# Kernel tuning notes

Measured on AMD Instinct MI355X. Metric: run time of the kernel, lower is better.

## Reference

```python
import jax, jax.numpy as jnp
import numpy as np

E, H, I = 5, 768, 1024  # num_experts, hidden_dim, intermediate_dim
TOP_K = 2


def setup_inputs() -> dict:
    key = jax.random.key(0)
    ks = jax.random.split(key, 6)
    s = 0.02
    return {
        "x": jax.random.normal(ks[0], (4, 2048, H), dtype=jnp.float32),
        "router_w": jax.random.normal(ks[1], (E, H), dtype=jnp.float32) * s,  # torch Linear (out,in)
        "router_b": jnp.zeros((E,), dtype=jnp.float32),
        "gate_w": jax.random.normal(ks[2], (E, H, I), dtype=jnp.float32) * s,
        "up_w": jax.random.normal(ks[3], (E, H, I), dtype=jnp.float32) * s,
        "down_w": jax.random.normal(ks[4], (E, I, H), dtype=jnp.float32) * s,
    }


def reference(x, router_w, router_b, gate_w, up_w, down_w):
    B, S, Hd = x.shape
    xf = x.reshape(-1, Hd)                       # [T, H]
    T = xf.shape[0]
    # Router: linear (with bias) -> softmax -> top-2 -> renormalize
    logits = xf @ router_w.T + router_b          # [T, E]
    scores = jax.nn.softmax(logits, axis=-1)
    vals, idx = jax.lax.top_k(scores, TOP_K)     # [T, 2]
    vals = vals / jnp.sum(vals, axis=-1, keepdims=True)
    # Dense combine weights: zero for unselected experts (same math as the
    # per-expert gather/scatter loop in the original module).
    comb = jnp.zeros((T, gate_w.shape[0]), dtype=x.dtype)
    comb = comb.at[jnp.arange(T)[:, None], idx].add(vals)  # [T, E]
    # SwiGLU per expert, vectorized over experts
    g = jnp.einsum('th,ehi->tei', xf, gate_w)    # [T, E, I]
    u = jnp.einsum('th,ehi->tei', xf, up_w)
    y = jnp.einsum('tei,eih->teh', jax.nn.silu(g) * u, down_w)  # [T, E, H]
    out = jnp.einsum('teh,te->th', y, comb)
    return out.reshape(B, S, Hd)
```

## Files before the change

### kernel.cpp

```cpp
#include <hip/hip_runtime.h>
#include <hip/hip_bf16.h>
#include <cstdint>
#include <cstddef>

#define T_TOK 8192
#define H_DIM 768
#define I_DIM 1024
#define N_EXP 5
#define MAXTILE 136

typedef short v8s __attribute__((ext_vector_type(8)));
typedef float v4f __attribute__((ext_vector_type(4)));

static __device__ __forceinline__ unsigned short f2bf(float f) {
    union { float f; unsigned int u; } v; v.f = f;
    unsigned int u = v.u;
    unsigned int r = (u + 0x7fffu + ((u >> 16) & 1u)) >> 16;
    return (unsigned short)r;
}
static __device__ __forceinline__ float bf2f(unsigned short s) {
    union { unsigned int u; float f; } v; v.u = ((unsigned int)s) << 16; return v.f;
}

static __device__ __forceinline__ void async16(const unsigned short* g, unsigned short* l) {
    __builtin_amdgcn_global_load_lds(
        (const __attribute__((address_space(1))) unsigned int*)g,
        (__attribute__((address_space(3))) unsigned int*)l, 16, 0, 0);
}

__global__ void k_prep(const float* __restrict__ gw, const float* __restrict__ uw,
                       const float* __restrict__ dw,
                       unsigned short* __restrict__ wbt, unsigned short* __restrict__ dbt,
                       const float* __restrict__ x, const float* __restrict__ rw,
                       const float* __restrict__ rb, unsigned short* __restrict__ xb,
                       int* __restrict__ top2e, float2* __restrict__ top2w) {
    const int z = blockIdx.z;
    const int tid = threadIdx.x;
    if (z < 3 * N_EXP) {
        __shared__ float tile[64][65];
        const int lrow = tid >> 4;
        const int lcol = (tid & 15) * 4;
        const int ocol = tid >> 2;
        const int seg = tid & 3;
        if (z < 2 * N_EXP) {
            if (blockIdx.y >= H_DIM / 64) return;
            const int e = z % N_EXP;
            const int isUp = z >= N_EXP;
            const float* src = (isUp ? uw : gw) + (size_t)e * H_DIM * I_DIM;
            const int c0 = blockIdx.x * 64, r0 = blockIdx.y * 64;
#pragma unroll
            for (int i = 0; i < 4; i++) {
                float4 v = *(const float4*)(src + (size_t)(r0 + i * 16 + lrow) * I_DIM + c0 + lcol);
                tile[i * 16 + lrow][lcol + 0] = v.x; tile[i * 16 + lrow][lcol + 1] = v.y;
                tile[i * 16 + lrow][lcol + 2] = v.z; tile[i * 16 + lrow][lcol + 3] = v.w;
            }
            __syncthreads();
            const int c = c0 + ocol;
            const int orow = (c >> 4) * 32 + (c & 15) + (isUp ? 16 : 0);
            unsigned short* dst = wbt + ((size_t)e * 2 * I_DIM + orow) * H_DIM + r0 + seg * 16;
#pragma unroll
            for (int q = 0; q < 4; q++) {
                ushort4 o;
                o.x = f2bf(tile[seg * 16 + q * 4 + 0][ocol]);
                o.y = f2bf(tile[seg * 16 + q * 4 + 1][ocol]);
                o.z = f2bf(tile[seg * 16 + q * 4 + 2][ocol]);
                o.w = f2bf(tile[seg * 16 + q * 4 + 3][ocol]);
                *(ushort4*)(dst + q * 4) = o;
            }
        } else {
            if (blockIdx.x >= H_DIM / 64) return;
            const int e = z - 2 * N_EXP;
            const float* src = dw + (size_t)e * I_DIM * H_DIM;
            unsigned short* dstb = dbt + (size_t)e * I_DIM * H_DIM;
            const int c0 = blockIdx.x * 64, r0 = blockIdx.y * 64;
#pragma unroll
            for (int i = 0; i < 4; i++) {
                float4 v = *(const float4*)(src + (size_t)(r0 + i * 16 + lrow) * H_DIM + c0 + lcol);
                tile[i * 16 + lrow][lcol + 0] = v.x; tile[i * 16 + lrow][lcol + 1] = v.y;
                tile[i * 16 + lrow][lcol + 2] = v.z; tile[i * 16 + lrow][lcol + 3] = v.w;
            }
            __syncthreads();
            const int c = c0 + ocol;
            unsigned short* dst = dstb + (size_t)c * I_DIM + r0 + seg * 16;
#pragma unroll
            for (int q = 0; q < 4; q++) {
                ushort4 o;
                o.x = f2bf(tile[seg * 16 + q * 4 + 0][ocol]);
                o.y = f2bf(tile[seg * 16 + q * 4 + 1][ocol]);
                o.z = f2bf(tile[seg * 16 + q * 4 + 2][ocol]);
                o.w = f2bf(tile[seg * 16 + q * 4 + 3][ocol]);
                *(ushort4*)(dst + q * 4) = o;
            }
        }
    } else {
        const int wave = tid >> 6, lane = tid & 63;
        const int b = (z - 3 * N_EXP) * 256 + blockIdx.y * 16 + blockIdx.x;
        const int t0 = b * 16 + wave * 4;
        float acc[4][N_EXP];
#pragma unroll
        for (int i = 0; i < 4; i++)
#pragma unroll
            for (int e = 0; e < N_EXP; e++) acc[i][e] = 0.f;
#pragma unroll
        for (int j = 0; j < H_DIM / 256; j++) {
            const int idx = j * 256 + lane * 4;
            float4 xv[4];
#pragma unroll
            for (int i = 0; i < 4; i++) {
                xv[i] = *(const float4*)(x + (size_t)(t0 + i) * H_DIM + idx);
                ushort4 o;
                o.x = f2bf(xv[i].x); o.y = f2bf(xv[i].y); o.z = f2bf(xv[i].z); o.w = f2bf(xv[i].w);
                *(ushort4*)(xb + (size_t)(t0 + i) * H_DIM + idx) = o;
            }
#pragma unroll
            for (int e = 0; e < N_EXP; e++) {
                float4 wv = *(const float4*)(rw + e * H_DIM + idx);
#pragma unroll
                for (int i = 0; i < 4; i++)
                    acc[i][e] += xv[i].x * wv.x + xv[i].y * wv.y + xv[i].z * wv.z + xv[i].w * wv.w;
            }
        }
#pragma unroll
        for (int s = 32; s > 0; s >>= 1) {
#pragma unroll
            for (int i = 0; i < 4; i++)
#pragma unroll
                for (int e = 0; e < N_EXP; e++) acc[i][e] += __shfl_down(acc[i][e], s);
        }
        if (lane == 0) {
#pragma unroll
            for (int i = 0; i < 4; i++) {
                float l[N_EXP];
#pragma unroll
                for (int e = 0; e < N_EXP; e++) l[e] = acc[i][e] + rb[e];
                int i1 = 0;
#pragma unroll
                for (int e = 1; e < N_EXP; e++) if (l[e] > l[i1]) i1 = e;
                int i2 = (i1 == 0) ? 1 : 0;
#pragma unroll
                for (int e = 0; e < N_EXP; e++) if (e != i1 && l[e] > l[i2]) i2 = e;
                float w1 = 1.f / (1.f + __expf(l[i2] - l[i1]));
                top2e[t0 + i] = i1 | (i2 << 8);
                top2w[t0 + i] = make_float2(w1, 1.f - w1);
            }
        }
    }
}

__global__ void k_router_b(const int* __restrict__ top2e, const float2* __restrict__ top2w,
                           int* __restrict__ cnt, int* __restrict__ tokslot,
                           float* __restrict__ pweight, int* __restrict__ done,
                           int4* __restrict__ tiles) {
    __shared__ int lcnt[N_EXP], lbase[N_EXP];
    const int tid = threadIdx.x;
    if (tid < N_EXP) lcnt[tid] = 0;
    __syncthreads();
    const int t = blockIdx.x * 256 + tid;
    const int pe = top2e[t];
    const float2 wv = top2w[t];
    const int e1 = pe & 0xff, e2 = pe >> 8;
    const int s1 = atomicAdd(&lcnt[e1], 1);
    const int s2 = atomicAdd(&lcnt[e2], 1);
    __syncthreads();
    if (tid < N_EXP) lbase[tid] = atomicAdd(&cnt[tid], lcnt[tid]);
    __syncthreads();
    const int p1 = lbase[e1] + s1;
    tokslot[e1 * T_TOK + p1] = t; pweight[e1 * T_TOK + p1] = wv.x;
    const int p2 = lbase[e2] + s2;
    tokslot[e2 * T_TOK + p2] = t | (1 << 16); pweight[e2 * T_TOK + p2] = wv.y;
    __syncthreads();
    if (tid == 0) {
        __threadfence();
        if (atomicAdd(done, 1) == (int)gridDim.x - 1) {
            int c[N_EXP], off = 0, idx = 0;
            for (int e = 0; e < N_EXP; e++) c[e] = atomicAdd(&cnt[e], 0);
            for (int e = 0; e < N_EXP; e++) {
                for (int m0 = 0; m0 < c[e]; m0 += 128)
                    tiles[idx++] = make_int4(e, m0, off, c[e]);
                off += c[e];
            }
            for (; idx < MAXTILE; idx++) tiles[idx] = make_int4(-1, 0, 0, 0);
        }
    }
}

__launch_bounds__(256, 4)
__global__ void k_gateup(const unsigned short* __restrict__ xb,
                         const unsigned short* __restrict__ wbt,
                         const int4* __restrict__ tiles,
                         const int* __restrict__ tokslot,
                         const float* __restrict__ pweight,
                         unsigned short* __restrict__ hbuf) {
    const int4 td = tiles[blockIdx.x];
    const int e = td.x;
    if (e < 0) return;
    const int m0 = td.y, offe = td.z, cn = td.w;
    const int n0 = blockIdx.y * 64;

    __shared__ __align__(16) unsigned short ldsA[128 * 64];
    __shared__ __align__(16) unsigned short ldsB[128 * 64];
    __shared__ int tokLds[128];
    __shared__ float pwLds[128];

    const int tid = threadIdx.x;
    if (tid < 128) {
        int gr = m0 + tid;
        int tk = 0; float pw = 0.f;
        if (gr < cn) { tk = tokslot[e * T_TOK + gr] & 0xFFFF; pw = pweight[e * T_TOK + gr]; }
        tokLds[tid] = tk; pwLds[tid] = pw;
    }
    __syncthreads();

    const int lane = tid & 63;
    const int wave = tid >> 6;
    const int fm = lane & 15, quad = lane >> 4;

    const int prow = lane >> 3;
    const int pc = lane & 7;
    const int lc8 = (pc ^ prow) * 8;

    unsigned aOff[4];
#pragma unroll
    for (int c = 0; c < 4; c++)
        aOff[c] = (unsigned)tokLds[c * 32 + wave * 8 + prow] * H_DIM;
    const unsigned short* aBase = xb + lc8;
    const unsigned short* bBase =
        wbt + ((size_t)e * 2 * I_DIM + n0 * 2 + wave * 8 + prow) * H_DIM + lc8;
    unsigned short* ldsAW = ldsA + wave * 8 * 64;
    unsigned short* ldsBW = ldsB + wave * 8 * 64;

    const int wm = (wave & 1) * 64, wnw = wave >> 1;

    v4f acc[4][4];
#pragma unroll
    for (int i = 0; i < 4; i++)
#pragma unroll
        for (int j = 0; j < 4; j++) acc[i][j] = (v4f)0.f;

    for (int kb = 0; kb < H_DIM / 64; kb++) {
        const int k0 = kb * 64;
#pragma unroll
        for (int c = 0; c < 4; c++)
            async16(aBase + aOff[c] + k0, ldsAW + c * 32 * 64);
#pragma unroll
        for (int c = 0; c < 4; c++)
            async16(bBase + (size_t)c * 32 * H_DIM + k0, ldsBW + c * 32 * 64);
        __syncthreads();
#pragma unroll
        for (int ks = 0; ks < 2; ks++) {
            const int pq = ((ks * 4 + quad) ^ (fm & 7)) * 8;
            v8s aF[4], bF[4];
#pragma unroll
            for (int im = 0; im < 4; im++)
                aF[im] = *(const v8s*)&ldsA[(wm + im * 16 + fm) * 64 + pq];
#pragma unroll
            for (int in = 0; in < 4; in++)
                bF[in] = *(const v8s*)&ldsB[(wnw * 64 + in * 16 + fm) * 64 + pq];
#pragma unroll
            for (int im = 0; im < 4; im++)
#pragma unroll
                for (int in = 0; in < 4; in++)
                    acc[im][in] = __builtin_amdgcn_mfma_f32_16x16x32_bf16(aF[im], bF[in], acc[im][in], 0, 0, 0);
        }
        __syncthreads();
    }

#pragma unroll
    for (int im = 0; im < 4; im++) {
#pragma unroll
        for (int reg = 0; reg < 4; reg++) {
            int lr = wm + im * 16 + quad * 4 + reg;
            int gr = m0 + lr;
            if (gr < cn) {
                float pw = pwLds[lr];
                size_t base = (size_t)(offe + gr) * I_DIM + n0 + wnw * 32 + fm;
#pragma unroll
                for (int j = 0; j < 2; j++) {
                    float g = acc[im][2 * j][reg];
                    float u = acc[im][2 * j + 1][reg];
                    float s = g / (1.f + __expf(-g));
                    hbuf[base + j * 16] = f2bf(s * u * pw);
                }
            }
        }
    }
}

__launch_bounds__(256, 4)
__global__ void k_down(const unsigned short* __restrict__ hbuf,
                       const unsigned short* __restrict__ dbt,
                       const int4* __restrict__ tiles,
                       const int* __restrict__ tokslot,
                       unsigned short* __restrict__ ybuf) {
    const int4 td = tiles[blockIdx.x];
    const int e = td.x;
    if (e < 0) return;
    const int m0 = td.y, offe = td.z, cn = td.w;
    const int n0 = blockIdx.y * 128;

    __shared__ __align__(16) unsigned short ldsA[128 * 64];
    __shared__ __align__(16) unsigned short ldsB[128 * 64];
    __shared__ int tokLds[128];

    const int tid = threadIdx.x;
    if (tid < 128) {
        int gr = m0 + tid;
        tokLds[tid] = (gr < cn) ? tokslot[e * T_TOK + gr] : 0;
    }
    __syncthreads();

    const int lane = tid & 63;
    const int wave = tid >> 6;
    const int fm = lane & 15, quad = lane >> 4;

    const int prow = lane >> 3;
    const int pc = lane & 7;
    const int lc8 = (pc ^ prow) * 8;

    unsigned aOff[4];
#pragma unroll
    for (int c = 0; c < 4; c++) {
        int ar = m0 + c * 32 + wave * 8 + prow;
        if (ar >= cn) ar = cn - 1;
        aOff[c] = (unsigned)(offe + ar) * I_DIM;
    }
    const unsigned short* aBase = hbuf + lc8;
    const unsigned short* bBase =
        dbt + ((size_t)e * H_DIM + n0 + wave * 8 + prow) * I_DIM + lc8;
    unsigned short* ldsAW = ldsA + wave * 8 * 64;
    unsigned short* ldsBW = ldsB + wave * 8 * 64;

    const int wm = (wave & 1) * 64, wn = (wave >> 1) * 64;

    v4f acc[4][4];
#pragma unroll
    for (int i = 0; i < 4; i++)
#pragma unroll
        for (int j = 0; j < 4; j++) acc[i][j] = (v4f)0.f;

    for (int kb = 0; kb < I_DIM / 64; kb++) {
        const int k0 = kb * 64;
#pragma unroll
        for (int c = 0; c < 4; c++)
            async16(aBase + aOff[c] + k0, ldsAW + c * 32 * 64);
#pragma unroll
        for (int c = 0; c < 4; c++)
            async16(bBase + (size_t)c * 32 * I_DIM + k0, ldsBW + c * 32 * 64);
        __syncthreads();
#pragma unroll
        for (int ks = 0; ks < 2; ks++) {
            const int pq = ((ks * 4 + quad) ^ (fm & 7)) * 8;
            v8s aF[4], bF[4];
#pragma unroll
            for (int im = 0; im < 4; im++)
                aF[im] = *(const v8s*)&ldsA[(wm + im * 16 + fm) * 64 + pq];
#pragma unroll
            for (int in = 0; in < 4; in++)
                bF[in] = *(const v8s*)&ldsB[(wn + in * 16 + fm) * 64 + pq];
#pragma unroll
            for (int im = 0; im < 4; im++)
#pragma unroll
                for (int in = 0; in < 4; in++)
                    acc[im][in] = __builtin_amdgcn_mfma_f32_16x16x32_bf16(aF[im], bF[in], acc[im][in], 0, 0, 0);
        }
        __syncthreads();
    }

#pragma unroll
    for (int im = 0; im < 4; im++) {
#pragma unroll
        for (int reg = 0; reg < 4; reg++) {
            int lr = wm + im * 16 + quad * 4 + reg;
            int gr = m0 + lr;
            if (gr < cn) {
                int v = tokLds[lr];
                int tok = v & 0xFFFF, s = (v >> 16) & 1;
#pragma unroll
                for (int in = 0; in < 4; in++) {
                    int col = n0 + wn + in * 16 + fm;
                    ybuf[((size_t)s * T_TOK + tok) * H_DIM + col] = f2bf(acc[im][in][reg]);
                }
            }
        }
    }
}

__global__ void k_combine(const unsigned short* __restrict__ ybuf, float* __restrict__ out) {
    const size_t i8 = ((size_t)blockIdx.x * 256 + threadIdx.x) * 8;
    const unsigned short* y0 = ybuf + i8;
    const unsigned short* y1 = ybuf + (size_t)T_TOK * H_DIM + i8;
    ushort4 a0 = *(const ushort4*)y0, a1 = *(const ushort4*)(y0 + 4);
    ushort4 b0 = *(const ushort4*)y1, b1 = *(const ushort4*)(y1 + 4);
    float4 o0, o1;
    o0.x = bf2f(a0.x) + bf2f(b0.x); o0.y = bf2f(a0.y) + bf2f(b0.y);
    o0.z = bf2f(a0.z) + bf2f(b0.z); o0.w = bf2f(a0.w) + bf2f(b0.w);
    o1.x = bf2f(a1.x) + bf2f(b1.x); o1.y = bf2f(a1.y) + bf2f(b1.y);
    o1.z = bf2f(a1.z) + bf2f(b1.z); o1.w = bf2f(a1.w) + bf2f(b1.w);
    *(float4*)(out + i8) = o0;
    *(float4*)(out + i8 + 4) = o1;
}

extern "C" void kernel_launch(void* const* d_in, const int* in_sizes, int n_in,
                              void* d_out, int out_size, void* d_ws, size_t ws_size,
                              hipStream_t stream) {
    const float* x  = (const float*)d_in[0];
    const float* rw = (const float*)d_in[1];
    const float* rb = (const float*)d_in[2];
    const float* gw = (const float*)d_in[3];
    const float* uw = (const float*)d_in[4];
    const float* dw = (const float*)d_in[5];
    float* out = (float*)d_out;

    char* ws = (char*)d_ws;
    size_t o = 0;
    auto alloc = [&](size_t bytes) { void* p = ws + o; o += (bytes + 255) & ~255ull; return p; };
    int*    cnt     = (int*)   alloc(8 * 4);
    int*    tokslot = (int*)   alloc((size_t)N_EXP * T_TOK * 4);
    float*  pweight = (float*) alloc((size_t)N_EXP * T_TOK * 4);
    int*    top2e   = (int*)   alloc((size_t)T_TOK * 4);
    float2* top2w   = (float2*)alloc((size_t)T_TOK * 8);
    int4*   tiles   = (int4*)  alloc((size_t)MAXTILE * 16);
    unsigned short* xb   = (unsigned short*)alloc((size_t)T_TOK * H_DIM * 2);
    unsigned short* wbt  = (unsigned short*)alloc((size_t)N_EXP * 2 * I_DIM * H_DIM * 2);
    unsigned short* dbt  = (unsigned short*)alloc((size_t)N_EXP * H_DIM * I_DIM * 2);
    unsigned short* hbuf = (unsigned short*)alloc((size_t)(2 * T_TOK + 128) * I_DIM * 2);
    unsigned short* ybuf = (unsigned short*)alloc((size_t)2 * T_TOK * H_DIM * 2);

    hipMemsetAsync(cnt, 0, 8 * 4, stream);

    dim3 pg(16, 16, 3 * N_EXP + 2);
    k_prep<<<pg, 256, 0, stream>>>(gw, uw, dw, wbt, dbt, x, rw, rb, xb, top2e, top2w);

    k_router_b<<<T_TOK / 256, 256, 0, stream>>>(top2e, top2w, cnt, tokslot, pweight,
                                                cnt + 5, tiles);

    dim3 g1(MAXTILE, I_DIM / 64);
    k_gateup<<<g1, 256, 0, stream>>>(xb, wbt, tiles, tokslot, pweight, hbuf);

    dim3 g2(MAXTILE, H_DIM / 128);
    k_down<<<g2, 256, 0, stream>>>(hbuf, dbt, tiles, tokslot, ybuf);

    k_combine<<<(T_TOK * H_DIM) / (256 * 8), 256, 0, stream>>>(ybuf, out);
}
```

Baseline: 240.3 us.

## Fuse gate-up, down and combine into one persistent work-queue megakernel

Replaces the separate gate/up GEMM, down GEMM and combine launches with one kernel whose blocks take work items from an atomic queue. Down-projection tiles wait on per-tile completion counters, and combine blocks wait on a global down counter, so down work for finished tiles can overlap the remaining gate/up work and launch gaps disappear. The cost is spin-waiting, acquire/release fences, and a fixed interleaving schedule that must avoid deadlock through in-order dispatch of work indices.

```diff
diff --git a/kernel.cpp b/kernel.cpp
--- a/kernel.cpp
+++ b/kernel.cpp
@@ -8,6 +8,14 @@
 #define I_DIM 1024
 #define N_EXP 5
 #define MAXTILE 136
+
+#define NGU (MAXTILE * 16)
+#define NDN (MAXTILE * 6)
+#define NCB 768
+#define QPRE 1024
+#define QG 72
+#define QMID (QG * 22)
+#define QD2 384
 
 typedef short v8s __attribute__((ext_vector_type(8)));
 typedef float v4f __attribute__((ext_vector_type(4)));
@@ -185,219 +193,248 @@
 }
 
 __launch_bounds__(256, 4)
-__global__ void k_gateup(const unsigned short* __restrict__ xb,
-                         const unsigned short* __restrict__ wbt,
-                         const int4* __restrict__ tiles,
-                         const int* __restrict__ tokslot,
-                         const float* __restrict__ pweight,
-                         unsigned short* __restrict__ hbuf) {
-    const int4 td = tiles[blockIdx.x];
-    const int e = td.x;
-    if (e < 0) return;
-    const int m0 = td.y, offe = td.z, cn = td.w;
-    const int n0 = blockIdx.y * 64;
-
+__global__ void k_mega(const unsigned short* __restrict__ xb,
+                       const unsigned short* __restrict__ wbt,
+                       const unsigned short* __restrict__ dbt,
+                       const int4* __restrict__ tiles,
+                       const int* __restrict__ tokslot,
+                       const float* __restrict__ pweight,
+                       unsigned short* __restrict__ hbuf,
+                       unsigned short* __restrict__ ybuf,
+                       float* __restrict__ out,
+                       int* __restrict__ qhead,
+                       int* __restrict__ gucnt,
+                       int* __restrict__ dncnt) {
     __shared__ __align__(16) unsigned short ldsA[128 * 64];
     __shared__ __align__(16) unsigned short ldsB[128 * 64];
     __shared__ int tokLds[128];
     __shared__ float pwLds[128];
+    __shared__ int widxS;
 
     const int tid = threadIdx.x;
-    if (tid < 128) {
-        int gr = m0 + tid;
-        int tk = 0; float pw = 0.f;
-        if (gr < cn) { tk = tokslot[e * T_TOK + gr] & 0xFFFF; pw = pweight[e * T_TOK + gr]; }
-        tokLds[tid] = tk; pwLds[tid] = pw;
+    if (tid == 0)
+        widxS = __hip_atomic_fetch_add(qhead, 1, __ATOMIC_RELAXED, __HIP_MEMORY_SCOPE_AGENT);
+    __syncthreads();
+    const int widx = widxS;
+
+    int role, item;
+    if (widx < QPRE) { role = 0; item = widx; }
+    else if (widx < QPRE + QMID) {
+        const int w2 = widx - QPRE, g = w2 / 22, r = w2 % 22;
+        if (r < 16) { role = 0; item = QPRE + g * 16 + r; }
+        else        { role = 1; item = g * 6 + (r - 16); }
+    } else if (widx < QPRE + QMID + QD2) {
+        role = 1; item = QG * 6 + (widx - (QPRE + QMID));
+    } else {
+        role = 2; item = widx - (QPRE + QMID + QD2);
     }
-    __syncthreads();
 
     const int lane = tid & 63;
     const int wave = tid >> 6;
     const int fm = lane & 15, quad = lane >> 4;
-
     const int prow = lane >> 3;
     const int pc = lane & 7;
     const int lc8 = (pc ^ prow) * 8;
 
-    unsigned aOff[4];
-#pragma unroll
-    for (int c = 0; c < 4; c++)
-        aOff[c] = (unsigned)tokLds[c * 32 + wave * 8 + prow] * H_DIM;
-    const unsigned short* aBase = xb + lc8;
-    const unsigned short* bBase =
-        wbt + ((size_t)e * 2 * I_DIM + n0 * 2 + wave * 8 + prow) * H_DIM + lc8;
-    unsigned short* ldsAW = ldsA + wave * 8 * 64;
-    unsigned short* ldsBW = ldsB + wave * 8 * 64;
-
-    const int wm = (wave & 1) * 64, wnw = wave >> 1;
-
-    v4f acc[4][4];
-#pragma unroll
-    for (int i = 0; i < 4; i++)
-#pragma unroll
-        for (int j = 0; j < 4; j++) acc[i][j] = (v4f)0.f;
-
-    for (int kb = 0; kb < H_DIM / 64; kb++) {
-        const int k0 = kb * 64;
-#pragma unroll
-        for (int c = 0; c < 4; c++)
-            async16(aBase + aOff[c] + k0, ldsAW + c * 32 * 64);
-#pragma unroll
-        for (int c = 0; c < 4; c++)
-            async16(bBase + (size_t)c * 32 * H_DIM + k0, ldsBW + c * 32 * 64);
+    if (role == 0) {
+        const int bx = item >> 4, by = item & 15;
+        const int4 td = tiles[bx];
+        const int e = td.x;
+        if (e >= 0) {
+            const int m0 = td.y, offe = td.z, cn = td.w;
+            const int n0 = by * 64;
+            if (tid < 128) {
+                int gr = m0 + tid;
+                int tk = 0; float pw = 0.f;
+                if (gr < cn) { tk = tokslot[e * T_TOK + gr] & 0xFFFF; pw = pweight[e * T_TOK + gr]; }
+                tokLds[tid] = tk; pwLds[tid] = pw;
+            }
+            __syncthreads();
+
+            unsigned aOff[4];
+#pragma unroll
+            for (int c = 0; c < 4; c++)
+                aOff[c] = (unsigned)tokLds[c * 32 + wave * 8 + prow] * H_DIM;
+            const unsigned short* aBase = xb + lc8;
+            const unsigned short* bBase =
+                wbt + ((size_t)e * 2 * I_DIM + n0 * 2 + wave * 8 + prow) * H_DIM + lc8;
+            unsigned short* ldsAW = ldsA + wave * 8 * 64;
+            unsigned short* ldsBW = ldsB + wave * 8 * 64;
+
+            const int wm = (wave & 1) * 64, wnw = wave >> 1;
+
+            v4f acc[4][4];
+#pragma unroll
+            for (int i = 0; i < 4; i++)
+#pragma unroll
+                for (int j = 0; j < 4; j++) acc[i][j] = (v4f)0.f;
+
+            for (int kb = 0; kb < H_DIM / 64; kb++) {
+                const int k0 = kb * 64;
+#pragma unroll
+                for (int c = 0; c < 4; c++)
+                    async16(aBase + aOff[c] + k0, ldsAW + c * 32 * 64);
+#pragma unroll
+                for (int c = 0; c < 4; c++)
+                    async16(bBase + (size_t)c * 32 * H_DIM + k0, ldsBW + c * 32 * 64);
+                __syncthreads();
+#pragma unroll
+                for (int ks = 0; ks < 2; ks++) {
+                    const int pq = ((ks * 4 + quad) ^ (fm & 7)) * 8;
+                    v8s aF[4], bF[4];
+#pragma unroll
+                    for (int im = 0; im < 4; im++)
+                        aF[im] = *(const v8s*)&ldsA[(wm + im * 16 + fm) * 64 + pq];
+#pragma unroll
+                    for (int in = 0; in < 4; in++)
+                        bF[in] = *(const v8s*)&ldsB[(wnw * 64 + in * 16 + fm) * 64 + pq];
+#pragma unroll
+                    for (int im = 0; im < 4; im++)
+#pragma unroll
+                        for (int in = 0; in < 4; in++)
+                            acc[im][in] = __builtin_amdgcn_mfma_f32_16x16x32_bf16(aF[im], bF[in], acc[im][in], 0, 0, 0);
+                }
+                __syncthreads();
+            }
+
+#pragma unroll
+            for (int im = 0; im < 4; im++) {
+#pragma unroll
+                for (int reg = 0; reg < 4; reg++) {
+                    int lr = wm + im * 16 + quad * 4 + reg;
+                    int gr = m0 + lr;
+                    if (gr < cn) {
+                        float pw = pwLds[lr];
+                        size_t base = (size_t)(offe + gr) * I_DIM + n0 + wnw * 32 + fm;
+#pragma unroll
+                        for (int j = 0; j < 2; j++) {
+                            float g = acc[im][2 * j][reg];
+                            float u = acc[im][2 * j + 1][reg];
+                            float s = g / (1.f + __expf(-g));
+                            hbuf[base + j * 16] = f2bf(s * u * pw);
+                        }
+                    }
+                }
+            }
+        }
         __syncthreads();
-#pragma unroll
-        for (int ks = 0; ks < 2; ks++) {
-            const int pq = ((ks * 4 + quad) ^ (fm & 7)) * 8;
-            v8s aF[4], bF[4];
-#pragma unroll
-            for (int im = 0; im < 4; im++)
-                aF[im] = *(const v8s*)&ldsA[(wm + im * 16 + fm) * 64 + pq];
-#pragma unroll
-            for (int in = 0; in < 4; in++)
-                bF[in] = *(const v8s*)&ldsB[(wnw * 64 + in * 16 + fm) * 64 + pq];
-#pragma unroll
-            for (int im = 0; im < 4; im++)
-#pragma unroll
-                for (int in = 0; in < 4; in++)
-                    acc[im][in] = __builtin_amdgcn_mfma_f32_16x16x32_bf16(aF[im], bF[in], acc[im][in], 0, 0, 0);
+        if (tid == 0)
+            __hip_atomic_fetch_add(&gucnt[bx], 1, __ATOMIC_RELEASE, __HIP_MEMORY_SCOPE_AGENT);
+    } else if (role == 1) {
+        const int bx = item / 6, by = item % 6;
+        if (tid == 0) {
+            while (__hip_atomic_load(&gucnt[bx], __ATOMIC_RELAXED, __HIP_MEMORY_SCOPE_AGENT) < 16)
+                __builtin_amdgcn_s_sleep(16);
         }
         __syncthreads();
+        __builtin_amdgcn_fence(__ATOMIC_ACQUIRE, "agent");
+
+        const int4 td = tiles[bx];
+        const int e = td.x;
+        if (e >= 0) {
+            const int m0 = td.y, offe = td.z, cn = td.w;
+            const int n0 = by * 128;
+            if (tid < 128) {
+                int gr = m0 + tid;
+                tokLds[tid] = (gr < cn) ? tokslot[e * T_TOK + gr] : 0;
+            }
+            __syncthreads();
+
+            unsigned aOff[4];
+#pragma unroll
+            for (int c = 0; c < 4; c++) {
+                int ar = m0 + c * 32 + wave * 8 + prow;
+                if (ar >= cn) ar = cn - 1;
+                aOff[c] = (unsigned)(offe + ar) * I_DIM;
+            }
+            const unsigned short* aBase = hbuf + lc8;
+            const unsigned short* bBase =
+                dbt + ((size_t)e * H_DIM + n0 + wave * 8 + prow) * I_DIM + lc8;
+            unsigned short* ldsAW = ldsA + wave * 8 * 64;
+            unsigned short* ldsBW = ldsB + wave * 8 * 64;
+
+            const int wm = (wave & 1) * 64, wn = (wave >> 1) * 64;
+
+            v4f acc[4][4];
+#pragma unroll
+            for (int i = 0; i < 4; i++)
+#pragma unroll
+                for (int j = 0; j < 4; j++) acc[i][j] = (v4f)0.f;
+
+            for (int kb = 0; kb < I_DIM / 64; kb++) {
+                const int k0 = kb * 64;
+#pragma unroll
+                for (int c = 0; c < 4; c++)
+                    async16(aBase + aOff[c] + k0, ldsAW + c * 32 * 64);
+#pragma unroll
+                for (int c = 0; c < 4; c++)
+                    async16(bBase + (size_t)c * 32 * I_DIM + k0, ldsBW + c * 32 * 64);
+                __syncthreads();
+#pragma unroll
+                for (int ks = 0; ks < 2; ks++) {
+                    const int pq = ((ks * 4 + quad) ^ (fm & 7)) * 8;
+                    v8s aF[4], bF[4];
+#pragma unroll
+                    for (int im = 0; im < 4; im++)
+                        aF[im] = *(const v8s*)&ldsA[(wm + im * 16 + fm) * 64 + pq];
+#pragma unroll
+                    for (int in = 0; in < 4; in++)
+                        bF[in] = *(const v8s*)&ldsB[(wn + in * 16 + fm) * 64 + pq];
+#pragma unroll
+                    for (int im = 0; im < 4; im++)
+#pragma unroll
+                        for (int in = 0; in < 4; in++)
+                            acc[im][in] = __builtin_amdgcn_mfma_f32_16x16x32_bf16(aF[im], bF[in], acc[im][in], 0, 0, 0);
+                }
+                __syncthreads();
+            }
+
+#pragma unroll
+            for (int im = 0; im < 4; im++) {
+#pragma unroll
+                for (int reg = 0; reg < 4; reg++) {
+                    int lr = wm + im * 16 + quad * 4 + reg;
+                    int gr = m0 + lr;
+                    if (gr < cn) {
+                        int v = tokLds[lr];
+                        int tok = v & 0xFFFF, s = (v >> 16) & 1;
+#pragma unroll
+                        for (int in = 0; in < 4; in++) {
+                            int col = n0 + wn + in * 16 + fm;
+                            ybuf[((size_t)s * T_TOK + tok) * H_DIM + col] = f2bf(acc[im][in][reg]);
+                        }
+                    }
+                }
+            }
+        }
+        __syncthreads();
+        if (tid == 0)
+            __hip_atomic_fetch_add(dncnt, 1, __ATOMIC_RELEASE, __HIP_MEMORY_SCOPE_AGENT);
+    } else {
+        if (tid == 0) {
+            while (__hip_atomic_load(dncnt, __ATOMIC_RELAXED, __HIP_MEMORY_SCOPE_AGENT) < NDN)
+                __builtin_amdgcn_s_sleep(32);
+        }
+        __syncthreads();
+        __builtin_amdgcn_fence(__ATOMIC_ACQUIRE, "agent");
+
+        const size_t base = (size_t)item * 8192;
+#pragma unroll
+        for (int it = 0; it < 4; ++it) {
+            const size_t i8 = base + (size_t)it * 2048 + tid * 8;
+            const unsigned short* y0 = ybuf + i8;
+            const unsigned short* y1 = ybuf + (size_t)T_TOK * H_DIM + i8;
+            ushort4 a0 = *(const ushort4*)y0, a1 = *(const ushort4*)(y0 + 4);
+            ushort4 b0 = *(const ushort4*)y1, b1 = *(const ushort4*)(y1 + 4);
+            float4 o0, o1;
+            o0.x = bf2f(a0.x) + bf2f(b0.x); o0.y = bf2f(a0.y) + bf2f(b0.y);
+            o0.z = bf2f(a0.z) + bf2f(b0.z); o0.w = bf2f(a0.w) + bf2f(b0.w);
+            o1.x = bf2f(a1.x) + bf2f(b1.x); o1.y = bf2f(a1.y) + bf2f(b1.y);
+            o1.z = bf2f(a1.z) + bf2f(b1.z); o1.w = bf2f(a1.w) + bf2f(b1.w);
+            *(float4*)(out + i8) = o0;
+            *(float4*)(out + i8 + 4) = o1;
+        }
     }
-
-#pragma unroll
-    for (int im = 0; im < 4; im++) {
-#pragma unroll
-        for (int reg = 0; reg < 4; reg++) {
-            int lr = wm + im * 16 + quad * 4 + reg;
-            int gr = m0 + lr;
-            if (gr < cn) {
-                float pw = pwLds[lr];
-                size_t base = (size_t)(offe + gr) * I_DIM + n0 + wnw * 32 + fm;
-#pragma unroll
-                for (int j = 0; j < 2; j++) {
-                    float g = acc[im][2 * j][reg];
-                    float u = acc[im][2 * j + 1][reg];
-                    float s = g / (1.f + __expf(-g));
-                    hbuf[base + j * 16] = f2bf(s * u * pw);
-                }
-            }
-        }
-    }
-}
-
-__launch_bounds__(256, 4)
-__global__ void k_down(const unsigned short* __restrict__ hbuf,
-                       const unsigned short* __restrict__ dbt,
-                       const int4* __restrict__ tiles,
-                       const int* __restrict__ tokslot,
-                       unsigned short* __restrict__ ybuf) {
-    const int4 td = tiles[blockIdx.x];
-    const int e = td.x;
-    if (e < 0) return;
-    const int m0 = td.y, offe = td.z, cn = td.w;
-    const int n0 = blockIdx.y * 128;
-
-    __shared__ __align__(16) unsigned short ldsA[128 * 64];
-    __shared__ __align__(16) unsigned short ldsB[128 * 64];
-    __shared__ int tokLds[128];
-
-    const int tid = threadIdx.x;
-    if (tid < 128) {
-        int gr = m0 + tid;
-        tokLds[tid] = (gr < cn) ? tokslot[e * T_TOK + gr] : 0;
-    }
-    __syncthreads();
-
-    const int lane = tid & 63;
-    const int wave = tid >> 6;
-    const int fm = lane & 15, quad = lane >> 4;
-
-    const int prow = lane >> 3;
-    const int pc = lane & 7;
-    const int lc8 = (pc ^ prow) * 8;
-
-    unsigned aOff[4];
-#pragma unroll
-    for (int c = 0; c < 4; c++) {
-        int ar = m0 + c * 32 + wave * 8 + prow;
-        if (ar >= cn) ar = cn - 1;
-        aOff[c] = (unsigned)(offe + ar) * I_DIM;
-    }
-    const unsigned short* aBase = hbuf + lc8;
-    const unsigned short* bBase =
-        dbt + ((size_t)e * H_DIM + n0 + wave * 8 + prow) * I_DIM + lc8;
-    unsigned short* ldsAW = ldsA + wave * 8 * 64;
-    unsigned short* ldsBW = ldsB + wave * 8 * 64;
-
-    const int wm = (wave & 1) * 64, wn = (wave >> 1) * 64;
-
-    v4f acc[4][4];
-#pragma unroll
-    for (int i = 0; i < 4; i++)
-#pragma unroll
-        for (int j = 0; j < 4; j++) acc[i][j] = (v4f)0.f;
-
-    for (int kb = 0; kb < I_DIM / 64; kb++) {
-        const int k0 = kb * 64;
-#pragma unroll
-        for (int c = 0; c < 4; c++)
-            async16(aBase + aOff[c] + k0, ldsAW + c * 32 * 64);
-#pragma unroll
-        for (int c = 0; c < 4; c++)
-            async16(bBase + (size_t)c * 32 * I_DIM + k0, ldsBW + c * 32 * 64);
-        __syncthreads();
-#pragma unroll
-        for (int ks = 0; ks < 2; ks++) {
-            const int pq = ((ks * 4 + quad) ^ (fm & 7)) * 8;
-            v8s aF[4], bF[4];
-#pragma unroll
-            for (int im = 0; im < 4; im++)
-                aF[im] = *(const v8s*)&ldsA[(wm + im * 16 + fm) * 64 + pq];
-#pragma unroll
-            for (int in = 0; in < 4; in++)
-                bF[in] = *(const v8s*)&ldsB[(wn + in * 16 + fm) * 64 + pq];
-#pragma unroll
-            for (int im = 0; im < 4; im++)
-#pragma unroll
-                for (int in = 0; in < 4; in++)
-                    acc[im][in] = __builtin_amdgcn_mfma_f32_16x16x32_bf16(aF[im], bF[in], acc[im][in], 0, 0, 0);
-        }
-        __syncthreads();
-    }
-
-#pragma unroll
-    for (int im = 0; im < 4; im++) {
-#pragma unroll
-        for (int reg = 0; reg < 4; reg++) {
-            int lr = wm + im * 16 + quad * 4 + reg;
-            int gr = m0 + lr;
-            if (gr < cn) {
-                int v = tokLds[lr];
-                int tok = v & 0xFFFF, s = (v >> 16) & 1;
-#pragma unroll
-                for (int in = 0; in < 4; in++) {
-                    int col = n0 + wn + in * 16 + fm;
-                    ybuf[((size_t)s * T_TOK + tok) * H_DIM + col] = f2bf(acc[im][in][reg]);
-                }
-            }
-        }
-    }
-}
-
-__global__ void k_combine(const unsigned short* __restrict__ ybuf, float* __restrict__ out) {
-    const size_t i8 = ((size_t)blockIdx.x * 256 + threadIdx.x) * 8;
-    const unsigned short* y0 = ybuf + i8;
-    const unsigned short* y1 = ybuf + (size_t)T_TOK * H_DIM + i8;
-    ushort4 a0 = *(const ushort4*)y0, a1 = *(const ushort4*)(y0 + 4);
-    ushort4 b0 = *(const ushort4*)y1, b1 = *(const ushort4*)(y1 + 4);
-    float4 o0, o1;
-    o0.x = bf2f(a0.x) + bf2f(b0.x); o0.y = bf2f(a0.y) + bf2f(b0.y);
-    o0.z = bf2f(a0.z) + bf2f(b0.z); o0.w = bf2f(a0.w) + bf2f(b0.w);
-    o1.x = bf2f(a1.x) + bf2f(b1.x); o1.y = bf2f(a1.y) + bf2f(b1.y);
-    o1.z = bf2f(a1.z) + bf2f(b1.z); o1.w = bf2f(a1.w) + bf2f(b1.w);
-    *(float4*)(out + i8) = o0;
-    *(float4*)(out + i8 + 4) = o1;
 }
 
 extern "C" void kernel_launch(void* const* d_in, const int* in_sizes, int n_in,
@@ -414,7 +451,7 @@
     char* ws = (char*)d_ws;
     size_t o = 0;
     auto alloc = [&](size_t bytes) { void* p = ws + o; o += (bytes + 255) & ~255ull; return p; };
-    int*    cnt     = (int*)   alloc(8 * 4);
+    int*    meta    = (int*)   alloc((8 + MAXTILE) * 4);
     int*    tokslot = (int*)   alloc((size_t)N_EXP * T_TOK * 4);
     float*  pweight = (float*) alloc((size_t)N_EXP * T_TOK * 4);
     int*    top2e   = (int*)   alloc((size_t)T_TOK * 4);
@@ -426,19 +463,15 @@
     unsigned short* hbuf = (unsigned short*)alloc((size_t)(2 * T_TOK + 128) * I_DIM * 2);
     unsigned short* ybuf = (unsigned short*)alloc((size_t)2 * T_TOK * H_DIM * 2);
 
-    hipMemsetAsync(cnt, 0, 8 * 4, stream);
+    hipMemsetAsync(meta, 0, (8 + MAXTILE) * 4, stream);
 
     dim3 pg(16, 16, 3 * N_EXP + 2);
     k_prep<<<pg, 256, 0, stream>>>(gw, uw, dw, wbt, dbt, x, rw, rb, xb, top2e, top2w);
 
-    k_router_b<<<T_TOK / 256, 256, 0, stream>>>(top2e, top2w, cnt, tokslot, pweight,
-                                                cnt + 5, tiles);
-
-    dim3 g1(MAXTILE, I_DIM / 64);
-    k_gateup<<<g1, 256, 0, stream>>>(xb, wbt, tiles, tokslot, pweight, hbuf);
-
-    dim3 g2(MAXTILE, H_DIM / 128);
-    k_down<<<g2, 256, 0, stream>>>(hbuf, dbt, tiles, tokslot, ybuf);
-
-    k_combine<<<(T_TOK * H_DIM) / (256 * 8), 256, 0, stream>>>(ybuf, out);
-}
+    k_router_b<<<T_TOK / 256, 256, 0, stream>>>(top2e, top2w, meta, tokslot, pweight,
+                                                meta + 5, tiles);
+
+    k_mega<<<NGU + NDN + NCB, 256, 0, stream>>>(xb, wbt, dbt, tiles, tokslot, pweight,
+                                                hbuf, ybuf, out,
+                                                meta + 6, meta + 8, meta + 7);
+}
```

Result: slower. 530.9 us (+120.9%).

## Fuse router scatter into prep kernel and drop LDS token staging in GEMMs

Applied to the files above, without the earlier changes.

Moves the per-expert slot assignment, token/weight scatter and tile-list construction into the router branch of the prep kernel, which removes one kernel launch and the top2e/top2w intermediate buffers. The gate-up and down GEMM kernels no longer stage token indices and weights in shared memory behind a barrier; they read tokslot/pweight directly from global memory. Launch bounds are raised from 4 to 5 blocks per SIMD to allow higher occupancy. The trade-offs are more scattered global loads in the epilogue and register pressure from the tighter launch bound.

```diff
diff --git a/kernel.cpp b/kernel.cpp
--- a/kernel.cpp
+++ b/kernel.cpp
@@ -8,6 +8,7 @@
 #define I_DIM 1024
 #define N_EXP 5
 #define MAXTILE 136
+#define NRBLK 512
 
 typedef short v8s __attribute__((ext_vector_type(8)));
 typedef float v4f __attribute__((ext_vector_type(4)));
@@ -33,7 +34,9 @@
                        unsigned short* __restrict__ wbt, unsigned short* __restrict__ dbt,
                        const float* __restrict__ x, const float* __restrict__ rw,
                        const float* __restrict__ rb, unsigned short* __restrict__ xb,
-                       int* __restrict__ top2e, float2* __restrict__ top2w) {
+                       int* __restrict__ cnt, int* __restrict__ tokslot,
+                       float* __restrict__ pweight, int* __restrict__ done,
+                       int4* __restrict__ tiles) {
     const int z = blockIdx.z;
     const int tid = threadIdx.x;
     if (z < 3 * N_EXP) {
@@ -93,9 +96,11 @@
             }
         }
     } else {
+        __shared__ int lcnt[N_EXP], lbase[N_EXP];
         const int wave = tid >> 6, lane = tid & 63;
         const int b = (z - 3 * N_EXP) * 256 + blockIdx.y * 16 + blockIdx.x;
         const int t0 = b * 16 + wave * 4;
+        if (tid < N_EXP) lcnt[tid] = 0;
         float acc[4][N_EXP];
 #pragma unroll
         for (int i = 0; i < 4; i++)
@@ -127,6 +132,9 @@
 #pragma unroll
                 for (int e = 0; e < N_EXP; e++) acc[i][e] += __shfl_down(acc[i][e], s);
         }
+        __syncthreads();
+        int se[8], sl[8], stok[8];
+        float swt[8];
         if (lane == 0) {
 #pragma unroll
             for (int i = 0; i < 4; i++) {
@@ -140,51 +148,42 @@
 #pragma unroll
                 for (int e = 0; e < N_EXP; e++) if (e != i1 && l[e] > l[i2]) i2 = e;
                 float w1 = 1.f / (1.f + __expf(l[i2] - l[i1]));
-                top2e[t0 + i] = i1 | (i2 << 8);
-                top2w[t0 + i] = make_float2(w1, 1.f - w1);
-            }
-        }
-    }
-}
-
-__global__ void k_router_b(const int* __restrict__ top2e, const float2* __restrict__ top2w,
-                           int* __restrict__ cnt, int* __restrict__ tokslot,
-                           float* __restrict__ pweight, int* __restrict__ done,
-                           int4* __restrict__ tiles) {
-    __shared__ int lcnt[N_EXP], lbase[N_EXP];
-    const int tid = threadIdx.x;
-    if (tid < N_EXP) lcnt[tid] = 0;
-    __syncthreads();
-    const int t = blockIdx.x * 256 + tid;
-    const int pe = top2e[t];
-    const float2 wv = top2w[t];
-    const int e1 = pe & 0xff, e2 = pe >> 8;
-    const int s1 = atomicAdd(&lcnt[e1], 1);
-    const int s2 = atomicAdd(&lcnt[e2], 1);
-    __syncthreads();
-    if (tid < N_EXP) lbase[tid] = atomicAdd(&cnt[tid], lcnt[tid]);
-    __syncthreads();
-    const int p1 = lbase[e1] + s1;
-    tokslot[e1 * T_TOK + p1] = t; pweight[e1 * T_TOK + p1] = wv.x;
-    const int p2 = lbase[e2] + s2;
-    tokslot[e2 * T_TOK + p2] = t | (1 << 16); pweight[e2 * T_TOK + p2] = wv.y;
-    __syncthreads();
-    if (tid == 0) {
-        __threadfence();
-        if (atomicAdd(done, 1) == (int)gridDim.x - 1) {
-            int c[N_EXP], off = 0, idx = 0;
-            for (int e = 0; e < N_EXP; e++) c[e] = atomicAdd(&cnt[e], 0);
-            for (int e = 0; e < N_EXP; e++) {
-                for (int m0 = 0; m0 < c[e]; m0 += 128)
-                    tiles[idx++] = make_int4(e, m0, off, c[e]);
-                off += c[e];
-            }
-            for (; idx < MAXTILE; idx++) tiles[idx] = make_int4(-1, 0, 0, 0);
-        }
-    }
-}
-
-__launch_bounds__(256, 4)
+                const int tok = t0 + i;
+                se[2 * i] = i1; stok[2 * i] = tok; swt[2 * i] = w1;
+                sl[2 * i] = atomicAdd(&lcnt[i1], 1);
+                se[2 * i + 1] = i2; stok[2 * i + 1] = tok | (1 << 16); swt[2 * i + 1] = 1.f - w1;
+                sl[2 * i + 1] = atomicAdd(&lcnt[i2], 1);
+            }
+        }
+        __syncthreads();
+        if (tid < N_EXP) lbase[tid] = atomicAdd(&cnt[tid], lcnt[tid]);
+        __syncthreads();
+        if (lane == 0) {
+#pragma unroll
+            for (int k = 0; k < 8; k++) {
+                const int p = lbase[se[k]] + sl[k];
+                tokslot[se[k] * T_TOK + p] = stok[k];
+                pweight[se[k] * T_TOK + p] = swt[k];
+            }
+        }
+        __syncthreads();
+        if (tid == 0) {
+            __threadfence();
+            if (atomicAdd(done, 1) == NRBLK - 1) {
+                int c[N_EXP], off = 0, idx = 0;
+                for (int e = 0; e < N_EXP; e++) c[e] = atomicAdd(&cnt[e], 0);
+                for (int e = 0; e < N_EXP; e++) {
+                    for (int m0 = 0; m0 < c[e]; m0 += 128)
+                        tiles[idx++] = make_int4(e, m0, off, c[e]);
+                    off += c[e];
+                }
+                for (; idx < MAXTILE; idx++) tiles[idx] = make_int4(-1, 0, 0, 0);
+            }
+        }
+    }
+}
+
+__launch_bounds__(256, 5)
 __global__ void k_gateup(const unsigned short* __restrict__ xb,
                          const unsigned short* __restrict__ wbt,
                          const int4* __restrict__ tiles,
@@ -199,18 +198,8 @@
 
     __shared__ __align__(16) unsigned short ldsA[128 * 64];
     __shared__ __align__(16) unsigned short ldsB[128 * 64];
-    __shared__ int tokLds[128];
-    __shared__ float pwLds[128];
 
     const int tid = threadIdx.x;
-    if (tid < 128) {
-        int gr = m0 + tid;
-        int tk = 0; float pw = 0.f;
-        if (gr < cn) { tk = tokslot[e * T_TOK + gr] & 0xFFFF; pw = pweight[e * T_TOK + gr]; }
-        tokLds[tid] = tk; pwLds[tid] = pw;
-    }
-    __syncthreads();
-
     const int lane = tid & 63;
     const int wave = tid >> 6;
     const int fm = lane & 15, quad = lane >> 4;
@@ -221,8 +210,11 @@
 
     unsigned aOff[4];
 #pragma unroll
-    for (int c = 0; c < 4; c++)
-        aOff[c] = (unsigned)tokLds[c * 32 + wave * 8 + prow] * H_DIM;
+    for (int c = 0; c < 4; c++) {
+        const int gr = m0 + c * 32 + wave * 8 + prow;
+        const int tk = (gr < cn) ? (tokslot[e * T_TOK + gr] & 0xFFFF) : 0;
+        aOff[c] = (unsigned)tk * H_DIM;
+    }
     const unsigned short* aBase = xb + lc8;
     const unsigned short* bBase =
         wbt + ((size_t)e * 2 * I_DIM + n0 * 2 + wave * 8 + prow) * H_DIM + lc8;
@@ -272,7 +264,7 @@
             int lr = wm + im * 16 + quad * 4 + reg;
             int gr = m0 + lr;
             if (gr < cn) {
-                float pw = pwLds[lr];
+                float pw = pweight[e * T_TOK + gr];
                 size_t base = (size_t)(offe + gr) * I_DIM + n0 + wnw * 32 + fm;
 #pragma unroll
                 for (int j = 0; j < 2; j++) {
@@ -286,7 +278,7 @@
     }
 }
 
-__launch_bounds__(256, 4)
+__launch_bounds__(256, 5)
 __global__ void k_down(const unsigned short* __restrict__ hbuf,
                        const unsigned short* __restrict__ dbt,
                        const int4* __restrict__ tiles,
@@ -300,15 +292,8 @@
 
     __shared__ __align__(16) unsigned short ldsA[128 * 64];
     __shared__ __align__(16) unsigned short ldsB[128 * 64];
-    __shared__ int tokLds[128];
 
     const int tid = threadIdx.x;
-    if (tid < 128) {
-        int gr = m0 + tid;
-        tokLds[tid] = (gr < cn) ? tokslot[e * T_TOK + gr] : 0;
-    }
-    __syncthreads();
-
     const int lane = tid & 63;
     const int wave = tid >> 6;
     const int fm = lane & 15, quad = lane >> 4;
@@ -373,7 +358,7 @@
             int lr = wm + im * 16 + quad * 4 + reg;
             int gr = m0 + lr;
             if (gr < cn) {
-                int v = tokLds[lr];
+                int v = tokslot[e * T_TOK + gr];
                 int tok = v & 0xFFFF, s = (v >> 16) & 1;
 #pragma unroll
                 for (int in = 0; in < 4; in++) {
@@ -417,8 +402,6 @@
     int*    cnt     = (int*)   alloc(8 * 4);
     int*    tokslot = (int*)   alloc((size_t)N_EXP * T_TOK * 4);
     float*  pweight = (float*) alloc((size_t)N_EXP * T_TOK * 4);
-    int*    top2e   = (int*)   alloc((size_t)T_TOK * 4);
-    float2* top2w   = (float2*)alloc((size_t)T_TOK * 8);
     int4*   tiles   = (int4*)  alloc((size_t)MAXTILE * 16);
     unsigned short* xb   = (unsigned short*)alloc((size_t)T_TOK * H_DIM * 2);
     unsigned short* wbt  = (unsigned short*)alloc((size_t)N_EXP * 2 * I_DIM * H_DIM * 2);
@@ -429,10 +412,8 @@
     hipMemsetAsync(cnt, 0, 8 * 4, stream);
 
     dim3 pg(16, 16, 3 * N_EXP + 2);
-    k_prep<<<pg, 256, 0, stream>>>(gw, uw, dw, wbt, dbt, x, rw, rb, xb, top2e, top2w);
-
-    k_router_b<<<T_TOK / 256, 256, 0, stream>>>(top2e, top2w, cnt, tokslot, pweight,
-                                                cnt + 5, tiles);
+    k_prep<<<pg, 256, 0, stream>>>(gw, uw, dw, wbt, dbt, x, rw, rb, xb,
+                                   cnt, tokslot, pweight, cnt + 5, tiles);
 
     dim3 g1(MAXTILE, I_DIM / 64);
     k_gateup<<<g1, 256, 0, stream>>>(xb, wbt, tiles, tokslot, pweight, hbuf);
```

Measured after the change: 278.6 us. +16.0%, slower.
